# Optimization experiments

Hardware: AMD Instinct MI355X
Metric: run time of the kernel (lower is better)

Reference implementation:

```python
import jax, jax.numpy as jnp
import numpy as np

B, S, D, H, EXP = 4, 2048, 768, 8, 4
HD = D // H  # head dim = 96
EPS = 1e-5


def layer_norm(x, g, b):
    mu = jnp.mean(x, axis=-1, keepdims=True)
    var = jnp.mean(jnp.square(x - mu), axis=-1, keepdims=True)
    return (x - mu) * jax.lax.rsqrt(var + EPS) * g + b


def setup_inputs() -> dict:
    key = jax.random.key(0)
    ks = jax.random.split(key, 16)
    s = 0.02
    f32 = jnp.float32
    x = jax.random.normal(ks[0], (B, S, D), f32)
    Wq = jax.random.normal(ks[1], (D, D), f32) * s
    bq = jnp.zeros((D,), f32)
    Wk = jax.random.normal(ks[2], (D, D), f32) * s
    bk = jnp.zeros((D,), f32)
    Wv = jax.random.normal(ks[3], (D, D), f32) * s
    bv = jnp.zeros((D,), f32)
    Wo = jax.random.normal(ks[4], (D, D), f32) * s
    bo = jnp.zeros((D,), f32)
    g1 = jnp.ones((D,), f32)
    be1 = jnp.zeros((D,), f32)
    W1 = jax.random.normal(ks[5], (D, D * EXP), f32) * s
    bf1 = jnp.zeros((D * EXP,), f32)
    W2 = jax.random.normal(ks[6], (D * EXP, D), f32) * s
    bf2 = jnp.zeros((D,), f32)
    g2 = jnp.ones((D,), f32)
    be2 = jnp.zeros((D,), f32)
    return dict(x=x, Wq=Wq, bq=bq, Wk=Wk, bk=bk, Wv=Wv, bv=bv, Wo=Wo, bo=bo,
                g1=g1, be1=be1, W1=W1, bf1=bf1, W2=W2, bf2=bf2, g2=g2, be2=be2)


def reference(x, Wq, bq, Wk, bk, Wv, bv, Wo, bo, g1, be1, W1, bf1, W2, bf2, g2, be2):
    scale = HD ** (-0.5)
    # multi-head attention (manual QK^T softmax V)
    q = (x @ Wq + bq).reshape(B, S, H, HD).transpose(0, 2, 1, 3)  # b H s c
    k = (x @ Wk + bk).reshape(B, S, H, HD).transpose(0, 2, 1, 3)
    v = (x @ Wv + bv).reshape(B, S, H, HD).transpose(0, 2, 1, 3)
    scores = jnp.einsum('bhqc,bhkc->bhqk', q, k) * scale
    attn = jax.nn.softmax(scores, axis=-1)
    o = jnp.einsum('bhqk,bhkc->bhqc', attn, v)
    o = o.transpose(0, 2, 1, 3).reshape(B, S, D)
    attn_out = o @ Wo + bo
    # residual + LN
    x1 = layer_norm(attn_out + x, g1, be1)
    # feed-forward with GELU
    h = jax.nn.gelu(x1 @ W1 + bf1)
    ffn_out = h @ W2 + bf2
    # residual + LN
    return layer_norm(ffn_out + x1, g2, be2)
```

## Files before the change

### kernel.cpp

```cpp
#include <hip/hip_runtime.h>
#include <hip/hip_bf16.h>
#include <math.h>
#include <stdint.h>

#define B_    4
#define S_    2048
#define D_    768
#define H_    8
#define HD_   96
#define EXPD_ 3072
#define MSZ   8192

#define QSCALE 0.14724439f
#define M0_    12.0f

typedef __bf16 bf16;
typedef __bf16 bf16x4 __attribute__((ext_vector_type(4)));
typedef __bf16 bf16x8 __attribute__((ext_vector_type(8)));
typedef float  f32x4  __attribute__((ext_vector_type(4)));
typedef float  f32x16 __attribute__((ext_vector_type(16)));

typedef __attribute__((address_space(1))) const uint32_t gu32;
typedef __attribute__((address_space(3))) uint32_t lu32;

__device__ __forceinline__ void async_copy16(const void* g, void* l) {
    __builtin_amdgcn_global_load_lds((gu32*)g, (lu32*)l, 16, 0, 0);
}

__device__ __forceinline__ float gelu_f(float x) {
    float x3 = x * x * x;
    return 0.5f * x * (1.0f + tanhf(0.7978845608028654f * (x + 0.044715f * x3)));
}

__device__ __forceinline__ bool sniff_f32(const void* p) {
    const bf16* pb = (const bf16*)p;
    float v = (float)pb[2 * (threadIdx.x & 63)];
    bool big = !(fabsf(v) < 1000.0f);
    return __any(big) != 0;
}

__device__ __forceinline__ float dynld(const void* p, size_t i, bool f32in) {
    return f32in ? ((const float*)p)[i] : (float)((const bf16*)p)[i];
}

__global__ __launch_bounds__(256) void cast_kernel(
    const void* __restrict__ src, bf16* __restrict__ dst)
{
    const bool f32in = sniff_f32(src);
    size_t i = ((size_t)blockIdx.x * 256 + threadIdx.x) * 8;
    if (f32in) {
        f32x4 a = *(const f32x4*)((const float*)src + i);
        f32x4 b = *(const f32x4*)((const float*)src + i + 4);
        bf16x8 r;
#pragma unroll
        for (int e = 0; e < 4; ++e) { r[e] = (bf16)a[e]; r[e + 4] = (bf16)b[e]; }
        *(bf16x8*)(dst + i) = r;
    } else {
        *(bf16x8*)(dst + i) = *(const bf16x8*)((const bf16*)src + i);
    }
}

#define MODE_QKV  0
#define MODE_RES  1
#define MODE_GELU 2

template<int MODE, bool ADYN, bool RESDYN, int BN>
__global__ __launch_bounds__(256) void gemm2_kernel(
    const void* __restrict__ A, const bf16* __restrict__ Bt,
    const void* __restrict__ b0, const void* __restrict__ b1, const void* __restrict__ b2,
    const void* __restrict__ res, bf16* __restrict__ out,
    int M, int N, int K, int ldb, int boff, const void* __restrict__ sniffp)
{
    constexpr int WN   = BN / 2;
    constexpr int NJ32 = WN / 32;
    __shared__ __align__(16) bf16 Sh[8192];
    bf16* As = Sh;
    bf16* Bs = Sh + 4096;

    const bool f32in = sniff_f32(sniffp);
    const int tid  = threadIdx.x;
    const int w    = tid >> 6;
    const int lane = tid & 63;
    const int l32  = lane & 31;
    const int kh   = lane >> 5;
    const int wr   = w >> 1, wc = w & 1;
    const int m0   = blockIdx.x * 128;
    const int n0   = blockIdx.y * BN;

    const int rsub = lane >> 2;
    const int cb8  = (lane & 3) * 8;

    f32x16 acc[2][NJ32];
#pragma unroll
    for (int i = 0; i < 2; ++i)
#pragma unroll
        for (int j = 0; j < NJ32; ++j)
#pragma unroll
            for (int e = 0; e < 16; ++e) acc[i][j][e] = 0.f;

    const bf16*  Abf = (const bf16*)A;
    const float* Af  = (const float*)A;

    for (int k0 = 0; k0 < K; k0 += 32) {
        __syncthreads();
        if (ADYN && f32in) {
#pragma unroll
            for (int a = 0; a < 2; ++a) {
                int row = w * 32 + a * 16 + rsub;
                const float* sp = Af + (size_t)(m0 + row) * K + k0 + cb8;
                f32x4 u0 = *(const f32x4*)sp;
                f32x4 u1 = *(const f32x4*)(sp + 4);
                bf16x8 v;
#pragma unroll
                for (int e = 0; e < 4; ++e) { v[e] = (bf16)u0[e]; v[e + 4] = (bf16)u1[e]; }
                *(bf16x8*)(&As[(size_t)(w * 32 + a * 16) * 32 + lane * 8]) = v;
            }
        } else {
#pragma unroll
            for (int a = 0; a < 2; ++a) {
                int row = w * 32 + a * 16 + rsub;
                async_copy16(Abf + (size_t)(m0 + row) * K + k0 + cb8,
                             &As[(w * 32 + a * 16) * 32]);
            }
        }
#pragma unroll
        for (int a = 0; a < BN / 64; ++a) {
            int row = w * (BN / 4) + a * 16 + rsub;
            async_copy16(Bt + (size_t)(n0 + row) * ldb + k0 + cb8,
                         &Bs[(w * (BN / 4) + a * 16) * 32]);
        }
        __syncthreads();

        bf16x8 af[2][2], bfv[NJ32][2];
#pragma unroll
        for (int i = 0; i < 2; ++i)
#pragma unroll
            for (int ks = 0; ks < 2; ++ks)
                af[i][ks] = *(const bf16x8*)(&As[(wr * 64 + i * 32 + l32) * 32 + ks * 16 + kh * 8]);
#pragma unroll
        for (int j = 0; j < NJ32; ++j)
#pragma unroll
            for (int ks = 0; ks < 2; ++ks)
                bfv[j][ks] = *(const bf16x8*)(&Bs[(wc * WN + j * 32 + l32) * 32 + ks * 16 + kh * 8]);
#pragma unroll
        for (int i = 0; i < 2; ++i)
#pragma unroll
            for (int j = 0; j < NJ32; ++j)
#pragma unroll
                for (int ks = 0; ks < 2; ++ks)
                    acc[i][j] = __builtin_amdgcn_mfma_f32_32x32x16_bf16(af[i][ks], bfv[j][ks], acc[i][j], 0, 0, 0);
    }

    if constexpr (MODE == MODE_QKV) {
#pragma unroll
        for (int j = 0; j < NJ32; ++j) {
            int nbase = n0 + wc * WN + j * 32;
            int which = nbase / D_;
            int n2b   = nbase - which * D_;
            int h     = n2b / HD_;
            int hd0   = n2b - h * HD_;
            const void* bp = which == 0 ? b0 : (which == 1 ? b1 : b2);
            float bval = dynld(bp, n2b + l32, f32in);
            int hd = hd0 + l32;
#pragma unroll
            for (int i = 0; i < 2; ++i) {
#pragma unroll
                for (int g = 0; g < 16; ++g) {
                    int rr = (g & 3) + 8 * (g >> 2) + 4 * kh;
                    int m  = m0 + wr * 64 + i * 32 + rr;
                    float v = acc[i][j][g] + bval;
                    int b  = m >> 11;
                    int ss = m & (S_ - 1);
                    int bh = b * H_ + h;
                    if (which == 0) v *= QSCALE;
                    size_t dst;
                    if (which < 2)
                        dst = (size_t)which * (MSZ * D_) + ((size_t)bh * S_ + ss) * HD_ + hd;
                    else
                        dst = (size_t)2 * (MSZ * D_) + ((size_t)bh * HD_ + hd) * S_ + ss;
                    out[dst] = (bf16)v;
                }
            }
        }
    } else {
        __syncthreads();
        bf16* Cw = Sh + w * 2048;
        for (int j = 0; j < NJ32; ++j) {
            int nl = n0 + wc * WN + j * 32 + l32;
            float bval = boff >= 0 ? dynld(b0, boff + nl, f32in) : 0.f;
#pragma unroll
            for (int i = 0; i < 2; ++i)
#pragma unroll
                for (int g = 0; g < 16; ++g) {
                    int rr = (g & 3) + 8 * (g >> 2) + 4 * kh;
                    float v = acc[i][j][g] + bval;
                    if constexpr (MODE == MODE_GELU) v = gelu_f(v);
                    Cw[(i * 32 + rr) * 32 + l32] = (bf16)v;
                }
#pragma unroll
            for (int pass = 0; pass < 4; ++pass) {
                int row = pass * 16 + (lane >> 2);
                int cc  = (lane & 3) * 8;
                bf16x8 cv = *(const bf16x8*)&Cw[row * 32 + cc];
                int m = m0 + wr * 64 + row;
                int n = n0 + wc * WN + j * 32 + cc;
                size_t off = (size_t)m * N + n;
                if constexpr (MODE == MODE_RES) {
                    bf16x8 o;
                    if (RESDYN && f32in) {
                        f32x4 r0 = *(const f32x4*)((const float*)res + off);
                        f32x4 r1 = *(const f32x4*)((const float*)res + off + 4);
#pragma unroll
                        for (int e = 0; e < 4; ++e) {
                            o[e]     = (bf16)((float)cv[e] + r0[e]);
                            o[e + 4] = (bf16)((float)cv[e + 4] + r1[e]);
                        }
                    } else {
                        bf16x8 rv = *(const bf16x8*)((const bf16*)res + off);
#pragma unroll
                        for (int e = 0; e < 8; ++e) o[e] = (bf16)((float)cv[e] + (float)rv[e]);
                    }
                    *(bf16x8*)&out[off] = o;
                } else {
                    *(bf16x8*)&out[off] = cv;
                }
            }
        }
    }
}

__global__ __launch_bounds__(512, 6) void flash_kernel(
    const bf16* __restrict__ Q, const bf16* __restrict__ Kk,
    const bf16* __restrict__ Vt_g, bf16* __restrict__ ctx)
{
    __shared__ __align__(16) bf16 Ks[64][104];
    __shared__ __align__(16) bf16 Vs[96][72];
    __shared__ __align__(16) bf16 Ps[8][16][72];

    const int tid  = threadIdx.x;
    const int w    = tid >> 6;
    const int lane = tid & 63;
    const int quad = lane >> 4;
    const int l16  = lane & 15;
    const int bh   = blockIdx.x;
    const size_t base = (size_t)bh * S_ * HD_;
    const int q0   = blockIdx.y * 128 + w * 16;

    bf16x8 qf[3];
#pragma unroll
    for (int ch = 0; ch < 3; ++ch)
        qf[ch] = *(const bf16x8*)(Q + base + (size_t)(q0 + l16) * HD_ + ch * 32 + quad * 8);

    f32x4 oacc[6];
#pragma unroll
    for (int c = 0; c < 6; ++c) oacc[c] = (f32x4){0.f, 0.f, 0.f, 0.f};
    float lsum[4] = {0.f, 0.f, 0.f, 0.f};

    const int kvi  = tid & 255;
    const int ch2  = tid >> 8;
    const int krow = kvi >> 2, kc8 = (kvi & 3) * 8 + ch2 * 32;
    const int vrow = (kvi >> 3) + ch2 * 32, vcb = (kvi & 7) * 8;
    const int krow2 = tid >> 2, kc82 = (tid & 3) * 8 + 64;
    const int vrow2 = (tid >> 3) + 64, vcb2 = (tid & 7) * 8;

    for (int kv0 = 0; kv0 < S_; kv0 += 64) {
        __syncthreads();
        *(bf16x8*)(&Ks[krow][kc8]) =
            *(const bf16x8*)(Kk + base + (size_t)(kv0 + krow) * HD_ + kc8);
        *(bf16x8*)(&Vs[vrow][vcb]) =
            *(const bf16x8*)(Vt_g + base + (size_t)vrow * S_ + kv0 + vcb);
        if (tid < 256) {
            *(bf16x8*)(&Ks[krow2][kc82]) =
                *(const bf16x8*)(Kk + base + (size_t)(kv0 + krow2) * HD_ + kc82);
            *(bf16x8*)(&Vs[vrow2][vcb2]) =
                *(const bf16x8*)(Vt_g + base + (size_t)vrow2 * S_ + kv0 + vcb2);
        }
        __syncthreads();

        f32x4 sacc[4];
#pragma unroll
        for (int t = 0; t < 4; ++t) {
            sacc[t] = (f32x4){0.f, 0.f, 0.f, 0.f};
#pragma unroll
            for (int ch = 0; ch < 3; ++ch) {
                bf16x8 kf = *(const bf16x8*)(&Ks[t * 16 + l16][ch * 32 + quad * 8]);
                sacc[t] = __builtin_amdgcn_mfma_f32_16x16x32_bf16(qf[ch], kf, sacc[t], 0, 0, 0);
            }
        }

#pragma unroll
        for (int r = 0; r < 4; ++r) {
            int qr = quad * 4 + r;
            float p0 = exp2f(sacc[0][r] - M0_);
            float p1 = exp2f(sacc[1][r] - M0_);
            float p2 = exp2f(sacc[2][r] - M0_);
            float p3 = exp2f(sacc[3][r] - M0_);
            lsum[r] += (p0 + p1) + (p2 + p3);
            Ps[w][qr][l16]      = (bf16)p0;
            Ps[w][qr][16 + l16] = (bf16)p1;
            Ps[w][qr][32 + l16] = (bf16)p2;
            Ps[w][qr][48 + l16] = (bf16)p3;
        }

        bf16x8 pf0 = *(const bf16x8*)(&Ps[w][l16][quad * 8]);
        bf16x8 pf1 = *(const bf16x8*)(&Ps[w][l16][32 + quad * 8]);
#pragma unroll
        for (int c = 0; c < 6; ++c) {
            bf16x8 vf0 = *(const bf16x8*)(&Vs[c * 16 + l16][quad * 8]);
            bf16x8 vf1 = *(const bf16x8*)(&Vs[c * 16 + l16][32 + quad * 8]);
            oacc[c] = __builtin_amdgcn_mfma_f32_16x16x32_bf16(pf0, vf0, oacc[c], 0, 0, 0);
            oacc[c] = __builtin_amdgcn_mfma_f32_16x16x32_bf16(pf1, vf1, oacc[c], 0, 0, 0);
        }
    }

#pragma unroll
    for (int r = 0; r < 4; ++r)
#pragma unroll
        for (int off = 1; off < 16; off <<= 1)
            lsum[r] += __shfl_xor(lsum[r], off);

    const int b = bh >> 3, h = bh & 7;
#pragma unroll
    for (int r = 0; r < 4; ++r) {
        float inv = 1.0f / lsum[r];
        int srow = q0 + quad * 4 + r;
        size_t rowbase = ((size_t)b * S_ + srow) * D_ + h * HD_;
#pragma unroll
        for (int c = 0; c < 6; ++c)
            ctx[rowbase + c * 16 + l16] = (bf16)(oacc[c][r] * inv);
    }
}

template<bool OUTDYN>
__global__ __launch_bounds__(256) void ln_kernel(
    const bf16* __restrict__ in, const void* __restrict__ g, const void* __restrict__ be,
    void* __restrict__ out, const void* __restrict__ sniffp)
{
    const bool f32in = sniff_f32(sniffp);
    const int w = threadIdx.x >> 6, lane = threadIdx.x & 63;
    const int row = blockIdx.x * 4 + w;
    const size_t rbase = (size_t)row * D_ + lane * 12;

    float v[12];
#pragma unroll
    for (int j = 0; j < 3; ++j) {
        bf16x4 t = *(const bf16x4*)(in + rbase + j * 4);
#pragma unroll
        for (int e = 0; e < 4; ++e) v[j * 4 + e] = (float)t[e];
    }
    float sum = 0.f;
#pragma unroll
    for (int j = 0; j < 12; ++j) sum += v[j];
#pragma unroll
    for (int off = 1; off < 64; off <<= 1) sum += __shfl_xor(sum, off);
    float mu = sum * (1.0f / D_);
    float sq = 0.f;
#pragma unroll
    for (int j = 0; j < 12; ++j) { v[j] -= mu; sq += v[j] * v[j]; }
#pragma unroll
    for (int off = 1; off < 64; off <<= 1) sq += __shfl_xor(sq, off);
    float rstd = rsqrtf(sq * (1.0f / D_) + 1e-5f);

    if (OUTDYN && f32in) {
        float* op = (float*)out + rbase;
#pragma unroll
        for (int j = 0; j < 3; ++j) {
            f32x4 t;
#pragma unroll
            for (int e = 0; e < 4; ++e) {
                int c = lane * 12 + j * 4 + e;
                t[e] = v[j * 4 + e] * rstd * dynld(g, c, true) + dynld(be, c, true);
            }
            *(f32x4*)(op + j * 4) = t;
        }
    } else {
        bf16* op = (bf16*)out + rbase;
#pragma unroll
        for (int j = 0; j < 3; ++j) {
            bf16x4 t;
#pragma unroll
            for (int e = 0; e < 4; ++e) {
                int c = lane * 12 + j * 4 + e;
                t[e] = (bf16)(v[j * 4 + e] * rstd * dynld(g, c, f32in) + dynld(be, c, f32in));
            }
            *(bf16x4*)(op + j * 4) = t;
        }
    }
}

__device__ __forceinline__ void transpose_tile(
    const void* __restrict__ src, bf16* __restrict__ dst, int R, int C,
    int r0, int c0, bool f32in)
{
    __shared__ bf16 t[64][65];
    const int tx = threadIdx.x & 63, ty = threadIdx.x >> 6;
#pragma unroll
    for (int i = 0; i < 16; ++i) {
        int rr = ty + i * 4;
        t[rr][tx] = (bf16)dynld(src, (size_t)(r0 + rr) * C + c0 + tx, f32in);
    }
    __syncthreads();
#pragma unroll
    for (int i = 0; i < 16; ++i) {
        int cc = ty + i * 4;
        dst[(size_t)(c0 + cc) * R + r0 + tx] = t[tx][cc];
    }
}

__global__ __launch_bounds__(256) void transpose_qkv_kernel(
    const void* __restrict__ s0, const void* __restrict__ s1, const void* __restrict__ s2,
    bf16* __restrict__ dst)
{
    const void* src = blockIdx.z == 0 ? s0 : (blockIdx.z == 1 ? s1 : s2);
    const bool f32in = sniff_f32(src);
    transpose_tile(src, dst + (size_t)blockIdx.z * D_ * D_, D_, D_,
                   blockIdx.y * 64, blockIdx.x * 64, f32in);
}

__global__ __launch_bounds__(256) void transpose_mlp_kernel(
    const void* __restrict__ s0, const void* __restrict__ s1, const void* __restrict__ s2,
    bf16* __restrict__ dst)
{
    int id = blockIdx.x;
    const void* src;
    int R, C, r, c;
    size_t off;
    if (id < 144)      { src = s0; R = D_;    C = D_;    off = 0;
                         r = id / 12;          c = id % 12; }
    else if (id < 720) { src = s1; R = D_;    C = EXPD_; off = (size_t)D_ * D_;
                         int i = id - 144;     r = i / 48; c = i % 48; }
    else               { src = s2; R = EXPD_; C = D_;    off = (size_t)D_ * D_ + (size_t)D_ * EXPD_;
                         int i = id - 720;     r = i / 12; c = i % 12; }
    const bool f32in = sniff_f32(src);
    transpose_tile(src, dst + off, R, C, r * 64, c * 64, f32in);
}

extern "C" void kernel_launch(void* const* d_in, const int* in_sizes, int n_in,
                              void* d_out, int out_size, void* d_ws, size_t ws_size,
                              hipStream_t stream)
{
    (void)in_sizes; (void)n_in; (void)out_size;
    const void* x   = d_in[0];
    const void* Wq  = d_in[1];
    const void* bq  = d_in[2];
    const void* Wk  = d_in[3];
    const void* bk  = d_in[4];
    const void* Wv  = d_in[5];
    const void* bv  = d_in[6];
    const void* Wo  = d_in[7];
    const void* bo  = d_in[8];
    const void* g1  = d_in[9];
    const void* be1 = d_in[10];
    const void* W1  = d_in[11];
    const void* bf1 = d_in[12];
    const void* W2  = d_in[13];
    const void* bf2 = d_in[14];
    const void* g2  = d_in[15];
    const void* be2 = d_in[16];

    const size_t REG = (size_t)MSZ * D_ * 2;
    char* p = (char*)d_ws;
    bf16* R0 = (bf16*)p;
    bf16* R1 = (bf16*)(p + REG);
    bf16* R2 = (bf16*)(p + 2 * REG);
    bf16* R3 = (bf16*)(p + 3 * REG);
    bf16* R4 = (bf16*)(p + 4 * REG);

    int tier = 0;
    if      (ws_size >= 9 * REG) tier = 3;
    else if (ws_size >= 5 * REG) tier = 1;
    bf16* xb = tier == 3 ? (bf16*)(p + 8 * REG) : R4;

    bf16* qkvT = (bf16*)d_out;
    bf16* ctx  = (bf16*)d_out;
    dim3 blk(256);

    if (tier >= 1) cast_kernel<<<dim3(MSZ * D_ / (256 * 8)), blk, 0, stream>>>(x, xb);

    transpose_qkv_kernel<<<dim3(12, 12, 3), blk, 0, stream>>>(Wq, Wk, Wv, qkvT);

    if (tier >= 1)
        gemm2_kernel<MODE_QKV, false, false, 128><<<dim3(MSZ / 128, 2304 / 128), blk, 0, stream>>>(
            xb, qkvT, bq, bk, bv, nullptr, R0, MSZ, 2304, D_, D_, 0, Wq);
    else
        gemm2_kernel<MODE_QKV, true, false, 128><<<dim3(MSZ / 128, 2304 / 128), blk, 0, stream>>>(
            x, qkvT, bq, bk, bv, nullptr, R0, MSZ, 2304, D_, D_, 0, Wq);

    flash_kernel<<<dim3(B_ * H_, S_ / 128), dim3(512), 0, stream>>>(R0, R1, R2, ctx);

    bf16* WoT = R1;
    bf16* W1T = WoT + (size_t)D_ * D_;
    bf16* W2T = W1T + (size_t)D_ * EXPD_;
    transpose_mlp_kernel<<<dim3(1296), blk, 0, stream>>>(Wo, W1, W2, WoT);

    if (tier >= 1)
        gemm2_kernel<MODE_RES, false, false, 64><<<dim3(MSZ / 128, D_ / 64), blk, 0, stream>>>(
            ctx, WoT, bo, nullptr, nullptr, xb, R3, MSZ, D_, D_, D_, 0, Wq);
    else
        gemm2_kernel<MODE_RES, false, true, 64><<<dim3(MSZ / 128, D_ / 64), blk, 0, stream>>>(
            ctx, WoT, bo, nullptr, nullptr, x, R3, MSZ, D_, D_, D_, 0, Wq);

    bf16* x1b = R0;
    ln_kernel<false><<<dim3(MSZ / 4), blk, 0, stream>>>(R3, g1, be1, x1b, Wq);

    bf16* y2b;
    if (tier == 3) {
        bf16* hb = R4;
        y2b = R3;
        gemm2_kernel<MODE_GELU, false, false, 128><<<dim3(MSZ / 128, EXPD_ / 128), blk, 0, stream>>>(
            x1b, W1T, bf1, nullptr, nullptr, nullptr, hb, MSZ, EXPD_, D_, D_, 0, Wq);
        gemm2_kernel<MODE_RES, false, false, 64><<<dim3(MSZ / 128, D_ / 64), blk, 0, stream>>>(
            hb, W2T, bf2, nullptr, nullptr, x1b, y2b, MSZ, D_, EXPD_, EXPD_, 0, Wq);
    } else if (tier == 1) {
        bf16* hb = R2;
        y2b = R4;
        gemm2_kernel<MODE_GELU, false, false, 128><<<dim3(MSZ / 128, 12), blk, 0, stream>>>(
            x1b, W1T, bf1, nullptr, nullptr, nullptr, hb, MSZ, 1536, D_, D_, 0, Wq);
        gemm2_kernel<MODE_RES, false, false, 64><<<dim3(MSZ / 128, D_ / 64), blk, 0, stream>>>(
            hb, W2T, bf2, nullptr, nullptr, x1b, y2b, MSZ, D_, 1536, EXPD_, 0, Wq);
        gemm2_kernel<MODE_GELU, false, false, 128><<<dim3(MSZ / 128, 12), blk, 0, stream>>>(
            x1b, W1T + (size_t)1536 * D_, bf1, nullptr, nullptr, nullptr, hb, MSZ, 1536, D_, D_, 1536, Wq);
        gemm2_kernel<MODE_RES, false, false, 64><<<dim3(MSZ / 128, D_ / 64), blk, 0, stream>>>(
            hb, W2T + 1536, nullptr, nullptr, nullptr, y2b, y2b, MSZ, D_, 1536, EXPD_, -1, Wq);
    } else {
        bf16* hb = R3;
        y2b = R2;
        const int CH = 2048;
        for (int c0 = 0; c0 < MSZ; c0 += CH) {
            const bf16* x1c = x1b + (size_t)c0 * D_;
            gemm2_kernel<MODE_GELU, false, false, 128><<<dim3(CH / 128, EXPD_ / 128), blk, 0, stream>>>(
                x1c, W1T, bf1, nullptr, nullptr, nullptr, hb, CH, EXPD_, D_, D_, 0, Wq);
            gemm2_kernel<MODE_RES, false, false, 64><<<dim3(CH / 128, D_ / 64), blk, 0, stream>>>(
                hb, W2T, bf2, nullptr, nullptr, x1c, y2b + (size_t)c0 * D_, CH, D_, EXPD_, EXPD_, 0, Wq);
        }
    }

    ln_kernel<true><<<dim3(MSZ / 4), blk, 0, stream>>>(y2b, g2, be2, d_out, Wq);
}
```

Before: 473.0 us.

## Remap GEMM tiles per XCD and split W2 GEMM along K into two passes

```diff
diff --git a/kernel.cpp b/kernel.cpp
--- a/kernel.cpp
+++ b/kernel.cpp
@@ -69,7 +69,8 @@
     const void* __restrict__ A, const bf16* __restrict__ Bt,
     const void* __restrict__ b0, const void* __restrict__ b1, const void* __restrict__ b2,
     const void* __restrict__ res, bf16* __restrict__ out,
-    int M, int N, int K, int ldb, int boff, const void* __restrict__ sniffp)
+    int M, int N, int K, int lda, int ldb, int boff, int mstripe,
+    const void* __restrict__ sniffp)
 {
     constexpr int WN   = BN / 2;
     constexpr int NJ32 = WN / 32;
@@ -84,8 +85,14 @@
     const int l32  = lane & 31;
     const int kh   = lane >> 5;
     const int wr   = w >> 1, wc = w & 1;
-    const int m0   = blockIdx.x * 128;
-    const int n0   = blockIdx.y * BN;
+
+    const int lin  = blockIdx.x;
+    const int xcd  = lin & 7;
+    const int q    = lin >> 3;
+    const int nb   = q / mstripe;
+    const int mbin = q - nb * mstripe;
+    const int m0   = (xcd * mstripe + mbin) * 128;
+    const int n0   = nb * BN;
 
     const int rsub = lane >> 2;
     const int cb8  = (lane & 3) * 8;
@@ -107,7 +114,7 @@
 #pragma unroll
             for (int a = 0; a < 2; ++a) {
                 int row = w * 32 + a * 16 + rsub;
-                const float* sp = Af + (size_t)(m0 + row) * K + k0 + cb8;
+                const float* sp = Af + (size_t)(m0 + row) * lda + k0 + cb8;
                 f32x4 u0 = *(const f32x4*)sp;
                 f32x4 u1 = *(const f32x4*)(sp + 4);
                 bf16x8 v;
@@ -119,7 +126,7 @@
 #pragma unroll
             for (int a = 0; a < 2; ++a) {
                 int row = w * 32 + a * 16 + rsub;
-                async_copy16(Abf + (size_t)(m0 + row) * K + k0 + cb8,
+                async_copy16(Abf + (size_t)(m0 + row) * lda + k0 + cb8,
                              &As[(w * 32 + a * 16) * 32]);
             }
         }
@@ -474,17 +481,18 @@
     bf16* qkvT = (bf16*)d_out;
     bf16* ctx  = (bf16*)d_out;
     dim3 blk(256);
+    const int MB8 = MSZ / 128 / 8;
 
     if (tier >= 1) cast_kernel<<<dim3(MSZ * D_ / (256 * 8)), blk, 0, stream>>>(x, xb);
 
     transpose_qkv_kernel<<<dim3(12, 12, 3), blk, 0, stream>>>(Wq, Wk, Wv, qkvT);
 
     if (tier >= 1)
-        gemm2_kernel<MODE_QKV, false, false, 128><<<dim3(MSZ / 128, 2304 / 128), blk, 0, stream>>>(
-            xb, qkvT, bq, bk, bv, nullptr, R0, MSZ, 2304, D_, D_, 0, Wq);
+        gemm2_kernel<MODE_QKV, false, false, 128><<<dim3(64 * 18), blk, 0, stream>>>(
+            xb, qkvT, bq, bk, bv, nullptr, R0, MSZ, 2304, D_, D_, D_, 0, MB8, Wq);
     else
-        gemm2_kernel<MODE_QKV, true, false, 128><<<dim3(MSZ / 128, 2304 / 128), blk, 0, stream>>>(
-            x, qkvT, bq, bk, bv, nullptr, R0, MSZ, 2304, D_, D_, 0, Wq);
+        gemm2_kernel<MODE_QKV, true, false, 128><<<dim3(64 * 18), blk, 0, stream>>>(
+            x, qkvT, bq, bk, bv, nullptr, R0, MSZ, 2304, D_, D_, D_, 0, MB8, Wq);
 
     flash_kernel<<<dim3(B_ * H_, S_ / 128), dim3(512), 0, stream>>>(R0, R1, R2, ctx);
 
@@ -494,11 +502,11 @@
     transpose_mlp_kernel<<<dim3(1296), blk, 0, stream>>>(Wo, W1, W2, WoT);
 
     if (tier >= 1)
-        gemm2_kernel<MODE_RES, false, false, 64><<<dim3(MSZ / 128, D_ / 64), blk, 0, stream>>>(
-            ctx, WoT, bo, nullptr, nullptr, xb, R3, MSZ, D_, D_, D_, 0, Wq);
+        gemm2_kernel<MODE_RES, false, false, 64><<<dim3(64 * 12), blk, 0, stream>>>(
+            ctx, WoT, bo, nullptr, nullptr, xb, R3, MSZ, D_, D_, D_, D_, 0, MB8, Wq);
     else
-        gemm2_kernel<MODE_RES, false, true, 64><<<dim3(MSZ / 128, D_ / 64), blk, 0, stream>>>(
-            ctx, WoT, bo, nullptr, nullptr, x, R3, MSZ, D_, D_, D_, 0, Wq);
+        gemm2_kernel<MODE_RES, false, true, 64><<<dim3(64 * 12), blk, 0, stream>>>(
+            ctx, WoT, bo, nullptr, nullptr, x, R3, MSZ, D_, D_, D_, D_, 0, MB8, Wq);
 
     bf16* x1b = R0;
     ln_kernel<false><<<dim3(MSZ / 4), blk, 0, stream>>>(R3, g1, be1, x1b, Wq);
@@ -507,31 +515,33 @@
     if (tier == 3) {
         bf16* hb = R4;
         y2b = R3;
-        gemm2_kernel<MODE_GELU, false, false, 128><<<dim3(MSZ / 128, EXPD_ / 128), blk, 0, stream>>>(
-            x1b, W1T, bf1, nullptr, nullptr, nullptr, hb, MSZ, EXPD_, D_, D_, 0, Wq);
-        gemm2_kernel<MODE_RES, false, false, 64><<<dim3(MSZ / 128, D_ / 64), blk, 0, stream>>>(
-            hb, W2T, bf2, nullptr, nullptr, x1b, y2b, MSZ, D_, EXPD_, EXPD_, 0, Wq);
+        gemm2_kernel<MODE_GELU, false, false, 128><<<dim3(64 * 24), blk, 0, stream>>>(
+            x1b, W1T, bf1, nullptr, nullptr, nullptr, hb, MSZ, EXPD_, D_, D_, D_, 0, MB8, Wq);
+        gemm2_kernel<MODE_RES, false, false, 64><<<dim3(64 * 12), blk, 0, stream>>>(
+            hb, W2T, bf2, nullptr, nullptr, x1b, y2b, MSZ, D_, 1536, EXPD_, EXPD_, 0, MB8, Wq);
+        gemm2_kernel<MODE_RES, false, false, 64><<<dim3(64 * 12), blk, 0, stream>>>(
+            hb + 1536, W2T + 1536, nullptr, nullptr, nullptr, y2b, y2b, MSZ, D_, 1536, EXPD_, EXPD_, -1, MB8, Wq);
     } else if (tier == 1) {
         bf16* hb = R2;
         y2b = R4;
-        gemm2_kernel<MODE_GELU, false, false, 128><<<dim3(MSZ / 128, 12), blk, 0, stream>>>(
-            x1b, W1T, bf1, nullptr, nullptr, nullptr, hb, MSZ, 1536, D_, D_, 0, Wq);
-        gemm2_kernel<MODE_RES, false, false, 64><<<dim3(MSZ / 128, D_ / 64), blk, 0, stream>>>(
-            hb, W2T, bf2, nullptr, nullptr, x1b, y2b, MSZ, D_, 1536, EXPD_, 0, Wq);
-        gemm2_kernel<MODE_GELU, false, false, 128><<<dim3(MSZ / 128, 12), blk, 0, stream>>>(
-            x1b, W1T + (size_t)1536 * D_, bf1, nullptr, nullptr, nullptr, hb, MSZ, 1536, D_, D_, 1536, Wq);
-        gemm2_kernel<MODE_RES, false, false, 64><<<dim3(MSZ / 128, D_ / 64), blk, 0, stream>>>(
-            hb, W2T + 1536, nullptr, nullptr, nullptr, y2b, y2b, MSZ, D_, 1536, EXPD_, -1, Wq);
+        gemm2_kernel<MODE_GELU, false, false, 128><<<dim3(64 * 12), blk, 0, stream>>>(
+            x1b, W1T, bf1, nullptr, nullptr, nullptr, hb, MSZ, 1536, D_, D_, D_, 0, MB8, Wq);
+        gemm2_kernel<MODE_RES, false, false, 64><<<dim3(64 * 12), blk, 0, stream>>>(
+            hb, W2T, bf2, nullptr, nullptr, x1b, y2b, MSZ, D_, 1536, 1536, EXPD_, 0, MB8, Wq);
+        gemm2_kernel<MODE_GELU, false, false, 128><<<dim3(64 * 12), blk, 0, stream>>>(
+            x1b, W1T + (size_t)1536 * D_, bf1, nullptr, nullptr, nullptr, hb, MSZ, 1536, D_, D_, D_, 1536, MB8, Wq);
+        gemm2_kernel<MODE_RES, false, false, 64><<<dim3(64 * 12), blk, 0, stream>>>(
+            hb, W2T + 1536, nullptr, nullptr, nullptr, y2b, y2b, MSZ, D_, 1536, 1536, EXPD_, -1, MB8, Wq);
     } else {
         bf16* hb = R3;
         y2b = R2;
         const int CH = 2048;
         for (int c0 = 0; c0 < MSZ; c0 += CH) {
             const bf16* x1c = x1b + (size_t)c0 * D_;
-            gemm2_kernel<MODE_GELU, false, false, 128><<<dim3(CH / 128, EXPD_ / 128), blk, 0, stream>>>(
-                x1c, W1T, bf1, nullptr, nullptr, nullptr, hb, CH, EXPD_, D_, D_, 0, Wq);
-            gemm2_kernel<MODE_RES, false, false, 64><<<dim3(CH / 128, D_ / 64), blk, 0, stream>>>(
-                hb, W2T, bf2, nullptr, nullptr, x1c, y2b + (size_t)c0 * D_, CH, D_, EXPD_, EXPD_, 0, Wq);
+            gemm2_kernel<MODE_GELU, false, false, 128><<<dim3(16 * 24), blk, 0, stream>>>(
+                x1c, W1T, bf1, nullptr, nullptr, nullptr, hb, CH, EXPD_, D_, D_, D_, 0, 2, Wq);
+            gemm2_kernel<MODE_RES, false, false, 64><<<dim3(16 * 12), blk, 0, stream>>>(
+                hb, W2T, bf2, nullptr, nullptr, x1c, y2b + (size_t)c0 * D_, CH, D_, EXPD_, EXPD_, EXPD_, 0, 2, Wq);
         }
     }
 
```

Result: no change. 478.8 us (+1.2%).
